# Kernel tuning notes

Hardware: AMD Instinct MI355X
Metric: run time of the kernel (lower is better)

## Reference

```python
import jax, jax.numpy as jnp
import numpy as np

N, T, D, H = 256, 512, 256, 256


def setup_inputs() -> dict:
    key = jax.random.key(0)
    ks = jax.random.split(key, 9)
    scale_x = float(np.sqrt(6.0 / (D + H)))  # xavier_uniform range approx
    scale_h = float(np.sqrt(6.0 / (H + H)))
    def wx(k):
        return jax.random.uniform(k, (D, H), jnp.float32, -scale_x, scale_x)
    def wh(k):
        return jax.random.uniform(k, (H, H), jnp.float32, -scale_h, scale_h)
    inp = {
        'x': jax.random.normal(ks[0], (N, T, D), jnp.float32),
        'w_ii': wx(ks[1]), 'w_hi': wh(ks[2]),
        'w_if': wx(ks[3]), 'w_hf': wh(ks[4]),
        'w_ig': wx(ks[5]), 'w_hg': wh(ks[6]),
        'w_io': wx(ks[7]), 'w_ho': wh(ks[8]),
        # init_hidden() zeros all 1-D params
        'b_ii': jnp.zeros((H,), jnp.float32), 'b_hi': jnp.zeros((H,), jnp.float32),
        'b_if': jnp.zeros((H,), jnp.float32), 'b_hf': jnp.zeros((H,), jnp.float32),
        'b_ig': jnp.zeros((H,), jnp.float32), 'b_hg': jnp.zeros((H,), jnp.float32),
        'b_io': jnp.zeros((H,), jnp.float32), 'b_ho': jnp.zeros((H,), jnp.float32),
    }
    return inp


def reference(x, w_ii, w_hi, w_if, w_hf, w_ig, w_hg, w_io, w_ho,
              b_ii, b_hi, b_if, b_hf, b_ig, b_hg, b_io, b_ho):
    # Fuse the 4 input projections and 4 hidden projections into 2 GEMMs
    # (mathematically identical to the 8 separate matmuls).
    Wx = jnp.concatenate([w_ii, w_if, w_ig, w_io], axis=1)  # (D, 4H)
    Wh = jnp.concatenate([w_hi, w_hf, w_hg, w_ho], axis=1)  # (H, 4H)
    b = jnp.concatenate([b_ii + b_hi, b_if + b_hf, b_ig + b_hg, b_io + b_ho])  # (4H,)
    n, t, _ = x.shape
    h = x.shape[2]  # noqa (not used)
    # Precompute input projections for all timesteps: (T, N, 4H)
    xW = jnp.einsum('ntd,dg->tng', x, Wx)
    h0 = jnp.zeros((n, w_hi.shape[0]), x.dtype)
    c0 = jnp.zeros_like(h0)

    def step(carry, xw_t):
        h_t, c_t = carry
        gates = xw_t + h_t @ Wh + b  # (N, 4H)
        i_t, f_t, g_t, o_t = jnp.split(gates, 4, axis=1)
        i_t = jax.nn.sigmoid(i_t)
        f_t = jax.nn.sigmoid(f_t)
        g_t = jnp.tanh(g_t)
        o_t = jax.nn.sigmoid(o_t)
        c_t = f_t * c_t + i_t * g_t
        h_t = o_t * jnp.tanh(c_t)
        return (h_t, c_t), None

    (h_T, c_T), _ = jax.lax.scan(step, (h0, c0), xW)
    return (h_T, c_T)
```

## Files before the change

### kernel.cpp

```cpp
#include <hip/hip_runtime.h>
#include <cstdint>

typedef float  f32x4  __attribute__((ext_vector_type(4)));
typedef __bf16 bf16x8 __attribute__((ext_vector_type(8)));
typedef int    i32x4  __attribute__((ext_vector_type(4)));
typedef unsigned short u16;
typedef u16 u16x4 __attribute__((ext_vector_type(4)));

#define TT 512

__device__ __forceinline__ u16 f2bf(float f) {
  unsigned u = __builtin_bit_cast(unsigned, f);
  unsigned r = u + 0x7fffu + ((u >> 16) & 1u);
  return (u16)(r >> 16);
}
__device__ __forceinline__ float bflo(unsigned d) { return __builtin_bit_cast(float, d << 16); }
__device__ __forceinline__ float bfhi(unsigned d) { return __builtin_bit_cast(float, d & 0xffff0000u); }
__device__ __forceinline__ float rcpf(float x) { return __builtin_amdgcn_rcpf(x); }
__device__ __forceinline__ float fsig(float x) { return rcpf(1.f + __expf(-x)); }
__device__ __forceinline__ float ftanh(float x) { return 1.f - 2.f * rcpf(1.f + __expf(2.f * x)); }
__device__ __forceinline__ void gload_lds16(const u16* g, u16* l) {
  __builtin_amdgcn_global_load_lds((const __attribute__((address_space(1))) void*)(g),
                                   (__attribute__((address_space(3))) void*)(l), 16, 0, 0);
}

__global__ __launch_bounds__(256) void prep_w(
    const float* __restrict__ wii, const float* __restrict__ whi,
    const float* __restrict__ wif, const float* __restrict__ whf,
    const float* __restrict__ wig, const float* __restrict__ whg,
    const float* __restrict__ wio, const float* __restrict__ who,
    const float* __restrict__ bii, const float* __restrict__ bhi,
    const float* __restrict__ bif, const float* __restrict__ bhf,
    const float* __restrict__ big_, const float* __restrict__ bhg,
    const float* __restrict__ bio, const float* __restrict__ bho,
    u16* __restrict__ Wxb, signed char* __restrict__ Whq,
    float* __restrict__ wscale, float* __restrict__ bsum) {
  __shared__ float red[256];
  int b = blockIdx.x;
  int tid = threadIdx.x;
  if (b < 1024) {
    const float* wx[4] = {wii, wif, wig, wio};
    int G = b >> 8, h = b & 255;
    Wxb[b * 256 + tid] = f2bf(wx[G][tid * 256 + h]);
  } else if (b < 2048) {
    const float* wh[4] = {whi, whf, whg, who};
    int cidx = b - 1024;
    int G = cidx >> 8, h = cidx & 255;
    float w = wh[G][tid * 256 + h];
    red[tid] = fabsf(w);
    __syncthreads();
    for (int s = 128; s > 0; s >>= 1) {
      if (tid < s) red[tid] = fmaxf(red[tid], red[tid + s]);
      __syncthreads();
    }
    float mx = red[0];
    float scale = (mx > 0.f) ? mx * (1.f / 127.f) : 1.f;
    float qf = rintf(w / scale);
    qf = fminf(127.f, fmaxf(-127.f, qf));
    Whq[cidx * 256 + tid] = (signed char)(int)qf;
    if (tid == 0) wscale[cidx] = scale * (1.f / 127.f);
  } else {
    const float* bx[4] = {bii, bif, big_, bio};
    const float* bh[4] = {bhi, bhf, bhg, bho};
    for (int G = 0; G < 4; ++G) bsum[G * 256 + tid] = bx[G][tid] + bh[G][tid];
  }
}

__global__ __launch_bounds__(512, 2) void lstm_fused(
    const float* __restrict__ X, const u16* __restrict__ Bt,
    const float* __restrict__ bias, const signed char* __restrict__ Whq,
    const float* __restrict__ wscale, u16* __restrict__ xWp,
    int* __restrict__ rprog, float* __restrict__ out) {
  __shared__ u16 As[128 * 256];
  __shared__ u16 Bp[128 * 256];
  __shared__ __align__(16) signed char hb[2][576];
  int p = blockIdx.x;
  int tid = threadIdx.x;

  if (p >= 128) {
    int k = p - 128;
    int l = tid & 63, w8 = tid >> 6;
    int wm = w8 >> 2, wn = w8 & 3;
    int c = l & 15, q = l >> 4;
    int sw = (c & 7) << 4;
    int rowbase[4];
#pragma unroll
    for (int mt = 0; mt < 4; ++mt) rowbase[mt] = (wm * 64 + mt * 16 + c) * 512;

#define STAGE_B(BN)                                                             \
    {                                                                           \
      _Pragma("unroll")                                                         \
      for (int s = 0; s < 8; ++s) {                                             \
        int i = s * 512 + tid;                                                  \
        int cl = i >> 5, wk = i & 31;                                           \
        gload_lds16(Bt + (size_t)((BN) * 128 + cl) * 256 +                      \
                        ((wk * 8) ^ ((cl & 7) << 3)),                           \
                    Bp + i * 8);                                                \
      }                                                                         \
    }

    for (int j = 0; j < 8; ++j) {
      int bm = j * 128 + k;
      __syncthreads();
      STAGE_B(0)
#pragma unroll 4
      for (int jj = 0; jj < 16; ++jj) {
        int row_l = jj * 8 + w8;
        int d = l * 4;
        int r = bm * 128 + row_l;
        int t = r >> 8, n = r & 255;
        const float4 v = *(const float4*)(X + ((size_t)n * 512 + t) * 256 + d);
        u16x4 pk;
        pk[0] = f2bf(v.x); pk[1] = f2bf(v.y); pk[2] = f2bf(v.z); pk[3] = f2bf(v.w);
        int ba = (row_l * 512 + l * 8) ^ ((row_l & 7) << 4);
        *(u16x4*)((char*)As + ba) = pk;
      }
      __syncthreads();

      f32x4 acc[4][2];
#pragma unroll
      for (int i = 0; i < 4; ++i)
#pragma unroll
        for (int jn = 0; jn < 2; ++jn) acc[i][jn] = (f32x4){0.f, 0.f, 0.f, 0.f};

      for (int bn = 0; bn < 8; ++bn) {
#pragma unroll
        for (int ko = 0; ko < 8; ++ko) {
          bf16x8 af[4], bfr[2];
          int koff = (ko * 64 + q * 16) ^ sw;
#pragma unroll
          for (int mt = 0; mt < 4; ++mt)
            af[mt] = *(const bf16x8*)((const char*)As + rowbase[mt] + koff);
#pragma unroll
          for (int nt = 0; nt < 2; ++nt)
            bfr[nt] = *(const bf16x8*)((const char*)Bp + (size_t)(wn * 32 + nt * 16 + c) * 512 + koff);
#pragma unroll
          for (int mt = 0; mt < 4; ++mt)
#pragma unroll
            for (int nt = 0; nt < 2; ++nt)
              acc[mt][nt] = __builtin_amdgcn_mfma_f32_16x16x32_bf16(af[mt], bfr[nt], acc[mt][nt], 0, 0, 0);
        }
#pragma unroll
        for (int mt = 0; mt < 4; ++mt) {
          int tm = bm * 8 + wm * 4 + mt;
#pragma unroll
          for (int nt = 0; nt < 2; ++nt) {
            int tn = bn * 8 + wn * 2 + nt;
            float bv = bias[tn * 16 + c];
            u16x4 pk;
#pragma unroll
            for (int r = 0; r < 4; ++r) pk[r] = f2bf(acc[mt][nt][r] + bv);
            *reinterpret_cast<u16x4*>(xWp + ((size_t)(tm * 64 + tn) * 256 + l * 4)) = pk;
            acc[mt][nt] = (f32x4){0.f, 0.f, 0.f, 0.f};
          }
        }
        if (bn < 7) {
          __syncthreads();
          STAGE_B(bn + 1)
          __syncthreads();
        }
      }
      __syncthreads();
      if (tid == 0)
        __hip_atomic_fetch_add(&rprog[j], 1, __ATOMIC_RELEASE, __HIP_MEMORY_SCOPE_AGENT);
    }
#undef STAGE_B
    return;
  }

  int xcd = p & 7, q8 = (p >> 3) & 7, tsel = p >> 6;
  int G = xcd * 2 + tsel;
  int wid = tid >> 6, l = tid & 63;
  int c = l & 15, q = (l >> 4) & 3;
  int tt = q >> 1, rsel = q & 1;

  for (int i = tid; i < 288; i += 512) ((int*)hb)[i] = 0;

  i32x4 bw[4][2][4];
#pragma unroll
  for (int g = 0; g < 4; ++g)
#pragma unroll
    for (int ttl = 0; ttl < 2; ++ttl) {
      int col = g * 256 + wid * 32 + ttl * 16 + c;
#pragma unroll
      for (int ks = 0; ks < 4; ++ks)
        bw[g][ttl][ks] = *reinterpret_cast<const i32x4*>(Whq + (size_t)col * 256 + ks * 64 + q * 16);
    }
  float sc8[4];
#pragma unroll
  for (int g = 0; g < 4; ++g) sc8[g] = wscale[g * 256 + wid * 32 + tt * 16 + c];

  const char* xbase = (const char*)xWp + (size_t)G * 32768;
  int xoff[4];
#pragma unroll
  for (int g = 0; g < 4; ++g) {
    int tn = g * 16 + wid * 2 + tt;
    xoff[g] = tn * 512 + (((q8 >> 1) * 16 + c) * 8) + (q8 & 1) * 4;
  }

  if (tid == 0) {
    while (__hip_atomic_load(&rprog[0], __ATOMIC_RELAXED, __HIP_MEMORY_SCOPE_AGENT) < 128)
      __builtin_amdgcn_s_sleep(8);
    (void)__hip_atomic_load(&rprog[0], __ATOMIC_ACQUIRE, __HIP_MEMORY_SCOPE_AGENT);
  }
  __syncthreads();

  unsigned xw0[4], xw1[4];
#pragma unroll
  for (int g = 0; g < 4; ++g) xw0[g] = *(const unsigned*)(xbase + xoff[g]);
  xbase += 524288;

  i32x4 zacc = (i32x4){0, 0, 0, 0};
  float cs = 0.f, hh = 0.f;
  __syncthreads();

#define STEP(CUR, XW_CUR, XW_NXT)                                               \
  {                                                                             \
    _Pragma("unroll")                                                           \
    for (int g = 0; g < 4; ++g) XW_NXT[g] = *(const unsigned*)(xbase + xoff[g]);\
    const signed char* hr = hb[CUR ^ 1];                                        \
    i32x4 acc[4][2];                                                            \
    {                                                                           \
      i32x4 a0 = *(const i32x4*)(hr + (c & 1) * 288 + q * 16);                  \
      _Pragma("unroll")                                                         \
      for (int g = 0; g < 4; ++g) {                                             \
        __asm__("v_mfma_i32_16x16x64_i8 %0, %1, %2, %3"                         \
                : "=&v"(acc[g][0]) : "v"(a0), "a"(bw[g][0][0]), "v"(zacc));     \
        __asm__("v_mfma_i32_16x16x64_i8 %0, %1, %2, %3"                         \
                : "=&v"(acc[g][1]) : "v"(a0), "a"(bw[g][1][0]), "v"(zacc));     \
      }                                                                         \
    }                                                                           \
    _Pragma("unroll")                                                           \
    for (int ks = 1; ks < 4; ++ks) {                                            \
      i32x4 a = *(const i32x4*)(hr + (c & 1) * 288 + ks * 64 + q * 16);         \
      _Pragma("unroll")                                                         \
      for (int g = 0; g < 4; ++g) {                                             \
        __asm__("v_mfma_i32_16x16x64_i8 %0, %1, %2, %0"                         \
                : "+v"(acc[g][0]) : "v"(a), "a"(bw[g][0][ks]));                 \
        __asm__("v_mfma_i32_16x16x64_i8 %0, %1, %2, %0"                         \
                : "+v"(acc[g][1]) : "v"(a), "a"(bw[g][1][ks]));                 \
      }                                                                         \
    }                                                                           \
    __asm__ volatile("s_nop 7\n\ts_nop 7\n\ts_nop 7");   \
    float a4[4];                                                                \
    _Pragma("unroll")                                                           \
    for (int g = 0; g < 4; ++g) {                                               \
      int e = tt ? (rsel ? acc[g][1][1] : acc[g][1][0])                         \
                 : (rsel ? acc[g][0][1] : acc[g][0][0]);                        \
      unsigned d = XW_CUR[g];                                                   \
      float xv = rsel ? bfhi(d) : bflo(d);                                      \
      a4[g] = (float)e * sc8[g] + xv;                                           \
    }                                                                           \
    float gi = fsig(a4[0]);                                                     \
    float gf = fsig(a4[1]);                                                     \
    float gg = ftanh(a4[2]);                                                    \
    float go = fsig(a4[3]);                                                     \
    cs = gf * cs + gi * gg;                                                     \
    hh = go * ftanh(cs);                                                        \
    int hq = (int)rintf(hh * 127.f);                                            \
    hb[CUR][rsel * 288 + wid * 32 + tt * 16 + c] = (signed char)hq;             \
    xbase += 524288;                                                            \
    __builtin_amdgcn_s_waitcnt(0xC07F);   \
    __builtin_amdgcn_s_barrier();                                               \
  }

  for (int t = 0; t < TT; t += 2) {
    STEP(0, xw0, xw1)
    if (((t + 2) & 63) == 0 && (t + 2) < TT) {
      int j = (t + 2) >> 6;
      if (tid == 0) {
        while (__hip_atomic_load(&rprog[j], __ATOMIC_RELAXED, __HIP_MEMORY_SCOPE_AGENT) < 128)
          __builtin_amdgcn_s_sleep(8);
        (void)__hip_atomic_load(&rprog[j], __ATOMIC_ACQUIRE, __HIP_MEMORY_SCOPE_AGENT);
      }
      __syncthreads();
    }
    STEP(1, xw1, xw0)
  }
#undef STEP

  {
    int n = G * 16 + q8 * 2 + rsel;
    int hu = wid * 32 + tt * 16 + c;
    out[(size_t)n * 256 + hu] = hh;
    out[65536 + (size_t)n * 256 + hu] = cs;
  }
}

extern "C" void kernel_launch(void* const* d_in, const int* in_sizes, int n_in,
                              void* d_out, int out_size, void* d_ws, size_t ws_size,
                              hipStream_t stream) {
  const float* x   = (const float*)d_in[0];
  const float* wii = (const float*)d_in[1];
  const float* whi = (const float*)d_in[2];
  const float* wif = (const float*)d_in[3];
  const float* whf = (const float*)d_in[4];
  const float* wig = (const float*)d_in[5];
  const float* whg = (const float*)d_in[6];
  const float* wio = (const float*)d_in[7];
  const float* who = (const float*)d_in[8];
  const float* bii = (const float*)d_in[9];
  const float* bhi = (const float*)d_in[10];
  const float* bif = (const float*)d_in[11];
  const float* bhf = (const float*)d_in[12];
  const float* big_ = (const float*)d_in[13];
  const float* bhg = (const float*)d_in[14];
  const float* bio = (const float*)d_in[15];
  const float* bho = (const float*)d_in[16];

  char* ws = (char*)d_ws;
  int*   rprog  = (int*)(ws);
  u16*   Wxb    = (u16*)(ws + 67108864);
  signed char* Whq = (signed char*)(ws + 67633152);
  float* wscale = (float*)(ws + 67895296);
  float* bsum   = (float*)(ws + 67899392);
  u16*   xWp    = (u16*)(ws + 67903488);
  float* out = (float*)d_out;

  hipMemsetAsync(rprog, 0, 64, stream);
  prep_w<<<2049, 256, 0, stream>>>(wii, whi, wif, whf, wig, whg, wio, who,
                                   bii, bhi, bif, bhf, big_, bhg, bio, bho,
                                   Wxb, Whq, wscale, bsum);
  lstm_fused<<<256, 512, 0, stream>>>(x, Wxb, bsum, Whq, wscale, xWp, rprog, out);
}
```

Before: 614.9 us.

## Double-buffer half-K B tiles in projection GEMM and tile-transpose weight prep

The projection-producer blocks now stage B in two half-K buffers and prefetch the next half while computing on the current one. This replaces the prior pattern of two barriers around a full-tile load with one barrier per half step, aiming to overlap global-to-LDS copies with MFMA work. Separately, the weight prep kernel moves from 2049 tiny blocks with strided column reads to 33 blocks that transpose through a padded shared tile. This gives coalesced reads and a cheaper abs-max reduction, but far fewer blocks run in parallel.

```diff
diff --git a/kernel.cpp b/kernel.cpp
--- a/kernel.cpp
+++ b/kernel.cpp
@@ -35,34 +35,70 @@
     const float* __restrict__ bio, const float* __restrict__ bho,
     u16* __restrict__ Wxb, signed char* __restrict__ Whq,
     float* __restrict__ wscale, float* __restrict__ bsum) {
+  __shared__ float tile[64][65];
   __shared__ float red[256];
+  __shared__ float scs[64];
   int b = blockIdx.x;
-  int tid = threadIdx.x;
-  if (b < 1024) {
+  int t = threadIdx.x;
+  int tlo = t & 63, thi = t >> 6;
+
+  if (b < 16) {
     const float* wx[4] = {wii, wif, wig, wio};
-    int G = b >> 8, h = b & 255;
-    Wxb[b * 256 + tid] = f2bf(wx[G][tid * 256 + h]);
-  } else if (b < 2048) {
+    int G = b >> 2, h0 = (b & 3) * 64;
+    const float* src = wx[G];
+    for (int dt = 0; dt < 4; ++dt) {
+#pragma unroll
+      for (int r = 0; r < 16; ++r) {
+        int dl = r * 4 + thi;
+        tile[dl][tlo] = src[(dt * 64 + dl) * 256 + h0 + tlo];
+      }
+      __syncthreads();
+#pragma unroll
+      for (int r = 0; r < 16; ++r) {
+        int hl = r * 4 + thi;
+        Wxb[(size_t)(G * 256 + h0 + hl) * 256 + dt * 64 + tlo] = f2bf(tile[tlo][hl]);
+      }
+      __syncthreads();
+    }
+  } else if (b < 32) {
     const float* wh[4] = {whi, whf, whg, who};
-    int cidx = b - 1024;
-    int G = cidx >> 8, h = cidx & 255;
-    float w = wh[G][tid * 256 + h];
-    red[tid] = fabsf(w);
+    int idx = b - 16;
+    int G = idx >> 2, h0 = (idx & 3) * 64;
+    const float* src = wh[G];
+    float am = 0.f;
+    for (int dd = 0; dd < 64; ++dd)
+      am = fmaxf(am, fabsf(src[(thi * 64 + dd) * 256 + h0 + tlo]));
+    red[t] = am;
     __syncthreads();
-    for (int s = 128; s > 0; s >>= 1) {
-      if (tid < s) red[tid] = fmaxf(red[tid], red[tid + s]);
-      __syncthreads();
-    }
-    float mx = red[0];
-    float scale = (mx > 0.f) ? mx * (1.f / 127.f) : 1.f;
-    float qf = rintf(w / scale);
-    qf = fminf(127.f, fmaxf(-127.f, qf));
-    Whq[cidx * 256 + tid] = (signed char)(int)qf;
-    if (tid == 0) wscale[cidx] = scale * (1.f / 127.f);
+    if (t < 64) {
+      float mx = fmaxf(fmaxf(red[t], red[t + 64]), fmaxf(red[t + 128], red[t + 192]));
+      float scale = (mx > 0.f) ? mx * (1.f / 127.f) : 1.f;
+      scs[t] = scale;
+      wscale[G * 256 + h0 + t] = scale * (1.f / 127.f);
+    }
+    __syncthreads();
+    for (int dt = 0; dt < 4; ++dt) {
+#pragma unroll
+      for (int r = 0; r < 16; ++r) {
+        int dl = r * 4 + thi;
+        tile[dl][tlo] = src[(dt * 64 + dl) * 256 + h0 + tlo];
+      }
+      __syncthreads();
+#pragma unroll
+      for (int r = 0; r < 16; ++r) {
+        int hl = r * 4 + thi;
+        float w = tile[tlo][hl];
+        float scale = scs[hl];
+        float qf = rintf(w / scale);
+        qf = fminf(127.f, fmaxf(-127.f, qf));
+        Whq[(size_t)(G * 256 + h0 + hl) * 256 + dt * 64 + tlo] = (signed char)(int)qf;
+      }
+      __syncthreads();
+    }
   } else {
     const float* bx[4] = {bii, bif, big_, bio};
     const float* bh[4] = {bhi, bhf, bhg, bho};
-    for (int G = 0; G < 4; ++G) bsum[G * 256 + tid] = bx[G][tid] + bh[G][tid];
+    for (int G = 0; G < 4; ++G) bsum[G * 256 + t] = bx[G][t] + bh[G][t];
   }
 }
 
@@ -72,7 +108,7 @@
     const float* __restrict__ wscale, u16* __restrict__ xWp,
     int* __restrict__ rprog, float* __restrict__ out) {
   __shared__ u16 As[128 * 256];
-  __shared__ u16 Bp[128 * 256];
+  __shared__ u16 Bh[2][128 * 128];
   __shared__ __align__(16) signed char hb[2][576];
   int p = blockIdx.x;
   int tid = threadIdx.x;
@@ -87,22 +123,22 @@
 #pragma unroll
     for (int mt = 0; mt < 4; ++mt) rowbase[mt] = (wm * 64 + mt * 16 + c) * 512;
 
-#define STAGE_B(BN)                                                             \
+#define STAGE_BH(BN, HALF, BUF)                                                 \
     {                                                                           \
       _Pragma("unroll")                                                         \
-      for (int s = 0; s < 8; ++s) {                                             \
-        int i = s * 512 + tid;                                                  \
-        int cl = i >> 5, wk = i & 31;                                           \
-        gload_lds16(Bt + (size_t)((BN) * 128 + cl) * 256 +                      \
+      for (int s2 = 0; s2 < 4; ++s2) {                                          \
+        int i = s2 * 512 + tid;                                                 \
+        int cl = i >> 4, wk = i & 15;                                           \
+        gload_lds16(Bt + (size_t)((BN) * 128 + cl) * 256 + (HALF) * 128 +       \
                         ((wk * 8) ^ ((cl & 7) << 3)),                           \
-                    Bp + i * 8);                                                \
+                    &Bh[BUF][0] + i * 8);                                       \
       }                                                                         \
     }
 
     for (int j = 0; j < 8; ++j) {
       int bm = j * 128 + k;
       __syncthreads();
-      STAGE_B(0)
+      STAGE_BH(0, 0, 0)
 #pragma unroll 4
       for (int jj = 0; jj < 16; ++jj) {
         int row_l = jj * 8 + w8;
@@ -123,48 +159,53 @@
 #pragma unroll
         for (int jn = 0; jn < 2; ++jn) acc[i][jn] = (f32x4){0.f, 0.f, 0.f, 0.f};
 
-      for (int bn = 0; bn < 8; ++bn) {
-#pragma unroll
-        for (int ko = 0; ko < 8; ++ko) {
+      for (int s = 0; s < 16; ++s) {
+        int bn = s >> 1, half = s & 1, buf = s & 1;
+        if (s < 15) {
+          int sn = s + 1;
+          STAGE_BH(sn >> 1, sn & 1, buf ^ 1)
+        }
+        const u16* bp = &Bh[buf][0];
+#pragma unroll
+        for (int kk = 0; kk < 4; ++kk) {
+          int ko = half * 4 + kk;
           bf16x8 af[4], bfr[2];
-          int koff = (ko * 64 + q * 16) ^ sw;
+          int koff  = (ko * 64 + q * 16) ^ sw;
+          int koffb = (kk * 64 + q * 16) ^ sw;
 #pragma unroll
           for (int mt = 0; mt < 4; ++mt)
             af[mt] = *(const bf16x8*)((const char*)As + rowbase[mt] + koff);
 #pragma unroll
           for (int nt = 0; nt < 2; ++nt)
-            bfr[nt] = *(const bf16x8*)((const char*)Bp + (size_t)(wn * 32 + nt * 16 + c) * 512 + koff);
+            bfr[nt] = *(const bf16x8*)((const char*)bp + (size_t)(wn * 32 + nt * 16 + c) * 256 + koffb);
 #pragma unroll
           for (int mt = 0; mt < 4; ++mt)
 #pragma unroll
             for (int nt = 0; nt < 2; ++nt)
               acc[mt][nt] = __builtin_amdgcn_mfma_f32_16x16x32_bf16(af[mt], bfr[nt], acc[mt][nt], 0, 0, 0);
         }
-#pragma unroll
-        for (int mt = 0; mt < 4; ++mt) {
-          int tm = bm * 8 + wm * 4 + mt;
-#pragma unroll
-          for (int nt = 0; nt < 2; ++nt) {
-            int tn = bn * 8 + wn * 2 + nt;
-            float bv = bias[tn * 16 + c];
-            u16x4 pk;
-#pragma unroll
-            for (int r = 0; r < 4; ++r) pk[r] = f2bf(acc[mt][nt][r] + bv);
-            *reinterpret_cast<u16x4*>(xWp + ((size_t)(tm * 64 + tn) * 256 + l * 4)) = pk;
-            acc[mt][nt] = (f32x4){0.f, 0.f, 0.f, 0.f};
+        if (half == 1) {
+#pragma unroll
+          for (int mt = 0; mt < 4; ++mt) {
+            int tm = bm * 8 + wm * 4 + mt;
+#pragma unroll
+            for (int nt = 0; nt < 2; ++nt) {
+              int tn = bn * 8 + wn * 2 + nt;
+              float bv = bias[tn * 16 + c];
+              u16x4 pk;
+#pragma unroll
+              for (int r = 0; r < 4; ++r) pk[r] = f2bf(acc[mt][nt][r] + bv);
+              *reinterpret_cast<u16x4*>(xWp + ((size_t)(tm * 64 + tn) * 256 + l * 4)) = pk;
+              acc[mt][nt] = (f32x4){0.f, 0.f, 0.f, 0.f};
+            }
           }
         }
-        if (bn < 7) {
-          __syncthreads();
-          STAGE_B(bn + 1)
-          __syncthreads();
-        }
-      }
-      __syncthreads();
+        __syncthreads();
+      }
       if (tid == 0)
         __hip_atomic_fetch_add(&rprog[j], 1, __ATOMIC_RELEASE, __HIP_MEMORY_SCOPE_AGENT);
     }
-#undef STAGE_B
+#undef STAGE_BH
     return;
   }
 
@@ -318,8 +359,8 @@
   float* out = (float*)d_out;
 
   hipMemsetAsync(rprog, 0, 64, stream);
-  prep_w<<<2049, 256, 0, stream>>>(wii, whi, wif, whf, wig, whg, wio, who,
-                                   bii, bhi, bif, bhf, big_, bhg, bio, bho,
-                                   Wxb, Whq, wscale, bsum);
+  prep_w<<<33, 256, 0, stream>>>(wii, whi, wif, whf, wig, whg, wio, who,
+                                 bii, bhi, bif, bhf, big_, bhg, bio, bho,
+                                 Wxb, Whq, wscale, bsum);
   lstm_fused<<<256, 512, 0, stream>>>(x, Wxb, bsum, Whq, wscale, xWp, rprog, out);
 }
```

Measured after the change: 641.1 us. 4.3% more time.
